# Kernel tuning notes

Hardware: AMD Instinct MI355X
Metric: run time of the kernel (lower is better)

Reference implementation:

```python
import jax, jax.numpy as jnp
import numpy as np

# ---- static config (matches init_kwargs) ----
B, L, C = 32, 512, 32
PRED = 96
D = 256
PS, STRIDE = 16, 8
P = (L - PS) // STRIDE + 1  # 63 patches
H = 4
DH = D // H                 # 64 per head
K = 4                        # causal conv kernel size
NB = 2                       # num sLSTM blocks
UP = 384                     # round_up(1.3 * 256, 64) gated-FFN inner dim


def setup_inputs() -> dict:
    key = jax.random.key(0)
    ks = iter(jax.random.split(key, 32))
    def nrm(shape, s=0.02):
        return jax.random.normal(next(ks), shape, dtype=jnp.float32) * s
    f32 = jnp.float32
    return dict(
        x=jax.random.normal(next(ks), (B, L, C), dtype=f32),
        W_emb=nrm((PS, D)), b_emb=jnp.zeros((D,), f32),
        ln1_w=jnp.ones((NB, D), f32), ln1_b=jnp.zeros((NB, D), f32),
        conv_w=nrm((NB, K, D), 0.1), conv_b=jnp.zeros((NB, D), f32),
        Wg=nrm((NB, 4, H, DH, DH), 0.05),   # input gate projections (i,f,z,o), block-diag per head
        Rg=nrm((NB, 4, H, DH, DH), 0.05),   # recurrent kernels per head
        gb=jnp.zeros((NB, 4, D), f32),      # gate biases
        gn_w=jnp.ones((NB, D), f32),        # per-head groupnorm weight
        ln2_w=jnp.ones((NB, D), f32), ln2_b=jnp.zeros((NB, D), f32),
        up_w=nrm((NB, D, 2 * UP)), up_b=jnp.zeros((NB, 2 * UP), f32),
        dn_w=nrm((NB, UP, D)), dn_b=jnp.zeros((NB, D), f32),
        post_w=jnp.ones((D,), f32), post_b=jnp.zeros((D,), f32),
        W_proj=nrm((D * P, PRED)), b_proj=jnp.zeros((PRED,), f32),
    )


def _layernorm(x, w, b, eps=1e-5):
    mu = x.mean(-1, keepdims=True)
    var = x.var(-1, keepdims=True)
    return (x - mu) / jnp.sqrt(var + eps) * w + b


def _slstm_layer(x, conv_w, conv_b, Wg, Rg, gb, gn_w):
    # x: (N, S, D)
    N, S, _ = x.shape
    # causal depthwise conv (k=K) + swish -> feeds i,f gates
    xp = jnp.pad(x, ((0, 0), (K - 1, 0), (0, 0)))
    xc = sum(xp[:, k:k + S, :] * conv_w[k] for k in range(K)) + conv_b
    xc = xc * jax.nn.sigmoid(xc)
    xh = x.reshape(N, S, H, DH)
    xch = xc.reshape(N, S, H, DH)
    gi = jnp.einsum('nshd,hde->nshe', xch, Wg[0]) + gb[0].reshape(H, DH)
    gf = jnp.einsum('nshd,hde->nshe', xch, Wg[1]) + gb[1].reshape(H, DH)
    gz = jnp.einsum('nshd,hde->nshe', xh, Wg[2]) + gb[2].reshape(H, DH)
    go = jnp.einsum('nshd,hde->nshe', xh, Wg[3]) + gb[3].reshape(H, DH)
    gates = jnp.moveaxis(jnp.stack([gi, gf, gz, go], 0), 2, 0)  # (S, 4, N, H, DH)

    def step(carry, g):
        c, n, h, m = carry  # each (N, H, DH)
        rec = jnp.einsum('nhd,ghde->gnhe', h, Rg)  # (4, N, H, DH)
        ip, fp, zp, op = g[0] + rec[0], g[1] + rec[1], g[2] + rec[2], g[3] + rec[3]
        logf = m + jax.nn.log_sigmoid(fp)          # log(f_t) + m_{t-1}
        m_new = jnp.maximum(ip, logf)              # stabilizer
        i = jnp.exp(ip - m_new)
        f = jnp.exp(logf - m_new)
        c_new = f * c + i * jnp.tanh(zp)
        n_new = f * n + i
        h_new = jax.nn.sigmoid(op) * c_new / n_new
        return (c_new, n_new, h_new, m_new), h_new

    z0 = jnp.zeros((N, H, DH), x.dtype)
    _, hs = jax.lax.scan(step, (z0, z0, z0, z0), gates)
    y = jnp.moveaxis(hs, 0, 1)  # (N, S, H, DH)
    mu = y.mean(-1, keepdims=True)
    var = y.var(-1, keepdims=True)
    y = (y - mu) / jnp.sqrt(var + 1e-5)            # per-head groupnorm
    return y.reshape(N, S, D) * gn_w


def reference(x, W_emb, b_emb, ln1_w, ln1_b, conv_w, conv_b, Wg, Rg, gb, gn_w,
              ln2_w, ln2_b, up_w, up_b, dn_w, dn_b, post_w, post_b, W_proj, b_proj):
    Bb, Ll, Cc = x.shape
    xs = x.transpose(0, 2, 1).reshape(Bb * Cc, Ll)              # (N, L)
    idx = np.arange(P)[:, None] * STRIDE + np.arange(PS)[None, :]
    patches = xs[:, idx]                                         # (N, P, PS) unfold
    h = patches @ W_emb + b_emb                                  # (N, P, D)
    for blk in range(NB):
        h = h + _slstm_layer(_layernorm(h, ln1_w[blk], ln1_b[blk]),
                             conv_w[blk], conv_b[blk], Wg[blk], Rg[blk], gb[blk], gn_w[blk])
        u = _layernorm(h, ln2_w[blk], ln2_b[blk]) @ up_w[blk] + up_b[blk]
        g1, g2 = jnp.split(u, 2, axis=-1)
        h = h + (jax.nn.gelu(g1) * g2) @ dn_w[blk] + dn_b[blk]   # gated FFN
    h = _layernorm(h, post_w, post_b)                            # post-blocks norm
    out = h.reshape(Bb * Cc, D * P) @ W_proj + b_proj            # (N, PRED)
    return out.reshape(Bb, Cc, PRED).transpose(0, 2, 1)          # (B, PRED, C)
```

## Files before the change

### kernel.cpp

```cpp
#include <hip/hip_runtime.h>
#include <stdint.h>

typedef unsigned short u16;
typedef unsigned int   u32;
typedef __attribute__((ext_vector_type(8))) short bf16x8;
typedef __attribute__((ext_vector_type(4))) float f32x4;

#define NS      63
#define NSEQ    1024
#define DDIM    256
#define NHEAD   4
#define DHEAD   64
#define UPDIM   384
#define PREDN   96
#define LLEN    512
#define CCH     32
#define PSIZE   16
#define PSTRIDE 8
#define KC_PROJ 8
#define KCHUNK_PROJ 2016

__device__ __forceinline__ float bf2f(u32 lo16){
  union { u32 i; float f; } v; v.i = lo16 << 16; return v.f;
}
__device__ __forceinline__ float bf2f_hi(u32 u){
  union { u32 i; float f; } v; v.i = u & 0xffff0000u; return v.f;
}
__device__ __forceinline__ u16 f2bf(float f){
  union { u32 i; float f; } v; v.f = f;
  u32 u = v.i; u += 0x7fffu + ((u >> 16) & 1u);
  return (u16)(u >> 16);
}

__device__ __forceinline__ void gload16(const u16* g, u16* lds){
  __builtin_amdgcn_global_load_lds(
      (const __attribute__((address_space(1))) u32*)g,
      (__attribute__((address_space(3))) u32*)lds, 16, 0, 0);
}

template<int N> __device__ __forceinline__ void waitcnt_vm(){
  if constexpr (N == 0) asm volatile("s_waitcnt vmcnt(0)" ::: "memory");
  else if constexpr (N == 4) asm volatile("s_waitcnt vmcnt(4)" ::: "memory");
  else if constexpr (N == 6) asm volatile("s_waitcnt vmcnt(6)" ::: "memory");
}

__device__ __forceinline__ void swz_tile(int &nt, int &mt){
  int gx = gridDim.x, gy = gridDim.y;
  int nwg = gx*gy;
  int flat = blockIdx.y*gx + blockIdx.x;
  int c = flat & 7, s = flat >> 3;
  int q = nwg >> 3, r = nwg & 7;
  int base = c*q + (c < r ? c : r);
  int t = base + s;
  nt = t % gx; mt = t / gx;
}

__global__ __launch_bounds__(256) void cvt_transpose_t(
    const float* __restrict__ src, u16* __restrict__ dst, int R, int C){
  __shared__ u16 tile[32][33];
  int rb = blockIdx.x*32, cb = blockIdx.y*32;
  int tx = threadIdx.x & 31, ty = threadIdx.x >> 5;
  #pragma unroll
  for (int i = ty; i < 32; i += 8){
    int r = rb + i, c = cb + tx;
    tile[i][tx] = (r < R && c < C) ? f2bf(src[(size_t)r*C + c]) : (u16)0;
  }
  __syncthreads();
  #pragma unroll
  for (int i = ty; i < 32; i += 8){
    int c = cb + i, r = rb + tx;
    if (c < C && r < R) dst[(size_t)c*R + r] = tile[tx][i];
  }
}

__global__ __launch_bounds__(256) void cvt_gate(
    const float* __restrict__ src, u16* __restrict__ dst){
  int mat = blockIdx.x, t = threadIdx.x;
  const float* s = src + (size_t)mat*4096;
  u16* d = dst + (size_t)mat*4096;
  for (int i = t; i < 4096; i += 256){
    int r = i >> 6, c = i & 63;
    d[c*64 + r] = f2bf(s[i]);
  }
}

__global__ __launch_bounds__(256) void cvt_gateW2(
    const float* __restrict__ Wg, u16* __restrict__ dst){
  int mi = blockIdx.x;
  int blk = mi >> 3, p = (mi >> 2) & 1, hd = mi & 3;
  u16* d = dst + (size_t)mi*8192;
  for (int i = threadIdx.x; i < 8192; i += 256){
    int n = i >> 6, k = i & 63;
    int e = n >> 1, gl = n & 1;
    int g = 2*p + gl;
    d[i] = f2bf(Wg[((((size_t)blk*4 + g)*4 + hd)*64 + k)*64 + e]);
  }
}

__global__ __launch_bounds__(256) void patch_embed_ln_v(
    const float* __restrict__ x, const float* __restrict__ Wemb,
    const float* __restrict__ bemb, const float* __restrict__ w1,
    const float* __restrict__ b1, u16* __restrict__ h,
    u16* __restrict__ outA, int t_base){
  int wv = blockIdx.x*4 + (threadIdx.x >> 6);
  int lane = threadIdx.x & 63;
  int tg = t_base + wv;
  int n = tg / NS, s = tg - n*NS;
  int b = n >> 5, c = n & 31;
  int l0 = s * PSTRIDE;
  float4 acc = *(const float4*)(bemb + lane*4);
  #pragma unroll
  for (int p = 0; p < PSIZE; ++p){
    float xv = x[((size_t)b*LLEN + l0 + p)*CCH + c];
    float4 we = *(const float4*)(Wemb + p*DDIM + lane*4);
    acc.x += xv*we.x; acc.y += xv*we.y; acc.z += xv*we.z; acc.w += xv*we.w;
  }
  ushort4 hu; hu.x=f2bf(acc.x); hu.y=f2bf(acc.y); hu.z=f2bf(acc.z); hu.w=f2bf(acc.w);
  *(ushort4*)(h + (size_t)wv*DDIM + lane*4) = hu;
  float s1 = acc.x+acc.y+acc.z+acc.w;
  float s2 = acc.x*acc.x+acc.y*acc.y+acc.z*acc.z+acc.w*acc.w;
  #pragma unroll
  for (int o = 1; o < 64; o <<= 1){ s1 += __shfl_xor(s1,o,64); s2 += __shfl_xor(s2,o,64); }
  float mu = s1*(1.f/DDIM);
  float var = s2*(1.f/DDIM) - mu*mu;
  float rstd = rsqrtf(var + 1e-5f);
  float4 wf = *(const float4*)(w1 + lane*4);
  float4 bf = *(const float4*)(b1 + lane*4);
  ushort4 o4;
  o4.x = f2bf((acc.x-mu)*rstd*wf.x + bf.x);
  o4.y = f2bf((acc.y-mu)*rstd*wf.y + bf.y);
  o4.z = f2bf((acc.z-mu)*rstd*wf.z + bf.z);
  o4.w = f2bf((acc.w-mu)*rstd*wf.w + bf.w);
  *(ushort4*)(outA + (size_t)wv*DDIM + lane*4) = o4;
}

__global__ __launch_bounds__(256) void layernorm_v(
    const u16* __restrict__ in, const float* __restrict__ w,
    const float* __restrict__ b, u16* __restrict__ out){
  int wv = blockIdx.x*4 + (threadIdx.x >> 6);
  int lane = threadIdx.x & 63;
  ushort4 u = *(const ushort4*)(in + (size_t)wv*DDIM + lane*4);
  float v0=bf2f(u.x), v1=bf2f(u.y), v2=bf2f(u.z), v3=bf2f(u.w);
  float s1 = v0+v1+v2+v3, s2 = v0*v0+v1*v1+v2*v2+v3*v3;
  #pragma unroll
  for (int o = 1; o < 64; o <<= 1){ s1 += __shfl_xor(s1,o,64); s2 += __shfl_xor(s2,o,64); }
  float mu = s1*(1.f/DDIM);
  float var = s2*(1.f/DDIM) - mu*mu;
  float rstd = rsqrtf(var + 1e-5f);
  float4 wf = *(const float4*)(w + lane*4);
  float4 bf = *(const float4*)(b + lane*4);
  ushort4 o4;
  o4.x = f2bf((v0-mu)*rstd*wf.x + bf.x);
  o4.y = f2bf((v1-mu)*rstd*wf.y + bf.y);
  o4.z = f2bf((v2-mu)*rstd*wf.z + bf.z);
  o4.w = f2bf((v3-mu)*rstd*wf.w + bf.w);
  *(ushort4*)(out + (size_t)wv*DDIM + lane*4) = o4;
}

__global__ __launch_bounds__(256) void gn_res_ln_v(
    const u16* __restrict__ y, const float* __restrict__ gnw,
    const float* __restrict__ w2, const float* __restrict__ b2,
    u16* __restrict__ h, u16* __restrict__ outA){
  int wv = blockIdx.x*4 + (threadIdx.x >> 6);
  int lane = threadIdx.x & 63;
  ushort4 u = *(const ushort4*)(y + (size_t)wv*DDIM + lane*4);
  float v0=bf2f(u.x), v1=bf2f(u.y), v2=bf2f(u.z), v3=bf2f(u.w);
  float s1 = v0+v1+v2+v3, s2 = v0*v0+v1*v1+v2*v2+v3*v3;
  #pragma unroll
  for (int o = 1; o < 16; o <<= 1){ s1 += __shfl_xor(s1,o,64); s2 += __shfl_xor(s2,o,64); }
  float mu64 = s1*(1.f/64.f);
  float var64 = s2*(1.f/64.f) - mu64*mu64;
  float rstd64 = rsqrtf(var64 + 1e-5f);
  float4 gw = *(const float4*)(gnw + lane*4);
  ushort4 hu = *(const ushort4*)(h + (size_t)wv*DDIM + lane*4);
  float h0 = bf2f(hu.x) + (v0-mu64)*rstd64*gw.x;
  float h1 = bf2f(hu.y) + (v1-mu64)*rstd64*gw.y;
  float h2 = bf2f(hu.z) + (v2-mu64)*rstd64*gw.z;
  float h3 = bf2f(hu.w) + (v3-mu64)*rstd64*gw.w;
  ushort4 hn; hn.x=f2bf(h0); hn.y=f2bf(h1); hn.z=f2bf(h2); hn.w=f2bf(h3);
  *(ushort4*)(h + (size_t)wv*DDIM + lane*4) = hn;
  float t1 = h0+h1+h2+h3, t2 = h0*h0+h1*h1+h2*h2+h3*h3;
  #pragma unroll
  for (int o = 1; o < 64; o <<= 1){ t1 += __shfl_xor(t1,o,64); t2 += __shfl_xor(t2,o,64); }
  float mu = t1*(1.f/DDIM);
  float var = t2*(1.f/DDIM) - mu*mu;
  float rstd = rsqrtf(var + 1e-5f);
  float4 wf = *(const float4*)(w2 + lane*4);
  float4 bf = *(const float4*)(b2 + lane*4);
  ushort4 o4;
  o4.x = f2bf((h0-mu)*rstd*wf.x + bf.x);
  o4.y = f2bf((h1-mu)*rstd*wf.y + bf.y);
  o4.z = f2bf((h2-mu)*rstd*wf.z + bf.z);
  o4.w = f2bf((h3-mu)*rstd*wf.w + bf.w);
  *(ushort4*)(outA + (size_t)wv*DDIM + lane*4) = o4;
}

__global__ __launch_bounds__(256) void conv_silu_v(
    const u16* __restrict__ xln, const float* __restrict__ cw,
    const float* __restrict__ cb, u16* __restrict__ xc){
  int wv = blockIdx.x*4 + (threadIdx.x >> 6);
  int lane = threadIdx.x & 63;
  int s = wv % NS;
  float4 acc = *(const float4*)(cb + lane*4);
  #pragma unroll
  for (int k = 0; k < 4; ++k){
    int ss = s + k - 3;
    if (ss >= 0){
      ushort4 xu = *(const ushort4*)(xln + (size_t)(wv + k - 3)*DDIM + lane*4);
      float4 cv = *(const float4*)(cw + k*DDIM + lane*4);
      acc.x += bf2f(xu.x)*cv.x; acc.y += bf2f(xu.y)*cv.y;
      acc.z += bf2f(xu.z)*cv.z; acc.w += bf2f(xu.w)*cv.w;
    }
  }
  ushort4 o4;
  o4.x = f2bf(acc.x/(1.f + __expf(-acc.x)));
  o4.y = f2bf(acc.y/(1.f + __expf(-acc.y)));
  o4.z = f2bf(acc.z/(1.f + __expf(-acc.z)));
  o4.w = f2bf(acc.w/(1.f + __expf(-acc.w)));
  *(ushort4*)(xc + (size_t)wv*DDIM + lane*4) = o4;
}

template<int BM,int BN,int WR,int WC,int MR,int NR,int MODE,int VM>
__global__ __launch_bounds__(256) void mfma_gemm2(
    const u16* __restrict__ A, int lda,
    const u16* __restrict__ Wt, int ldwt,
    const float* __restrict__ bias, void* __restrict__ outp, int ldo,
    int ksteps, int kchunk, int Mtot)
{
  constexpr int nA = BM/16, nW = BN/16;
  __shared__ u16 As[2][BM*32];
  __shared__ u16 Ws[2][BN*32];
  const int tid = threadIdx.x;
  const int lane = tid & 63, wid = tid >> 6;
  const int wr = wid / WC, wc = wid % WC;
  const int fr = lane & 15, kb = lane >> 4;
  int nt, mt; swz_tile(nt, mt);
  const int m0 = mt*BM, n0 = nt*BN;
  const int kc = blockIdx.z;
  const int kbeg = kc*kchunk;
  const u16* Ab = A + (size_t)m0*lda + kbeg;
  const u16* Wb = Wt + (size_t)n0*ldwt + kbeg;
  const int lrow = lane >> 2;
  const int lcol = (((lane & 3) ^ (lrow & 3)) * 8);
  const int rsw = (kb ^ (fr & 3))*8;

  auto stage = [&](int buf, int ks){
    int k0 = ks*32;
    for (int c = wid; c < nA; c += 4)
      gload16(Ab + (size_t)(c*16 + lrow)*lda + k0 + lcol, &As[buf][c*512]);
    for (int c = wid; c < nW; c += 4)
      gload16(Wb + (size_t)(c*16 + lrow)*ldwt + k0 + lcol, &Ws[buf][c*512]);
  };

  f32x4 acc[MR][NR];
  #pragma unroll
  for (int m=0;m<MR;++m)
    #pragma unroll
    for (int n=0;n<NR;++n) acc[m][n] = (f32x4){0.f,0.f,0.f,0.f};

  stage(0, 0);
  if (VM == 0) __syncthreads();
  int cur = 0;
  for (int ks = 0; ks < ksteps; ++ks){
    if (VM == 0){
      if (ks + 1 < ksteps) stage(cur^1, ks+1);
    } else {
      if (ks + 1 < ksteps){ stage(cur^1, ks+1); waitcnt_vm<VM>(); }
      else waitcnt_vm<0>();
      __builtin_amdgcn_s_barrier();
      asm volatile("" ::: "memory");
    }
    bf16x8 af[MR], wf[NR];
    #pragma unroll
    for (int m=0;m<MR;++m)
      af[m] = *(const bf16x8*)&As[cur][(wr*MR*16 + m*16 + fr)*32 + rsw];
    #pragma unroll
    for (int n=0;n<NR;++n)
      wf[n] = *(const bf16x8*)&Ws[cur][(wc*NR*16 + n*16 + fr)*32 + rsw];
    #pragma unroll
    for (int m=0;m<MR;++m)
      #pragma unroll
      for (int n=0;n<NR;++n)
        acc[m][n] = __builtin_amdgcn_mfma_f32_16x16x32_bf16(af[m], wf[n], acc[m][n], 0,0,0);
    if (VM == 0){
      __syncthreads();
    } else {
      asm volatile("" ::: "memory");
      __builtin_amdgcn_s_barrier();
    }
    cur ^= 1;
  }
  #pragma unroll
  for (int m=0;m<MR;++m){
    int rowb = m0 + wr*MR*16 + m*16 + kb*4;
    #pragma unroll
    for (int n=0;n<NR;++n){
      int col = n0 + wc*NR*16 + n*16 + fr;
      #pragma unroll
      for (int r=0;r<4;++r){
        int row = rowb + r;
        float v = acc[m][n][r];
        if (MODE == 1){
          u16* dst = (u16*)outp + (size_t)row*ldo + col;
          *dst = f2bf(bf2f(*dst) + v + bias[col]);
        } else {
          ((float*)outp)[((size_t)kc*Mtot + row)*ldo + col] = v;
        }
      }
    }
  }
}

__global__ __launch_bounds__(256) void mfma_gate2(
    const u16* __restrict__ xc, const u16* __restrict__ xh,
    const u16* __restrict__ Wg2, const float* __restrict__ gb,
    u16* __restrict__ gates)
{
  __shared__ u16 As[2][128*32];
  __shared__ u16 Ws[2][128*32];
  const int tid = threadIdx.x;
  const int lane = tid & 63, wid = tid >> 6;
  const int wr = wid >> 1, wc = wid & 1;
  const int fr = lane & 15, kb = lane >> 4;
  int nt, mt; swz_tile(nt, mt);
  const int p = nt >> 2, hd = nt & 3;
  const int m0 = mt*128;
  const u16* Ain = (p == 0) ? xc : xh;
  const u16* Wb = Wg2 + (size_t)nt*8192;
  const int lrow = lane >> 2;
  const int lcol = (((lane & 3) ^ (lrow & 3)) * 8);
  const int rsw = (kb ^ (fr & 3))*8;

  auto stage = [&](int buf, int ks){
    int k0 = ks*32;
    for (int c = wid; c < 8; c += 4)
      gload16(Ain + (size_t)(m0 + c*16 + lrow)*DDIM + hd*64 + k0 + lcol, &As[buf][c*512]);
    for (int c = wid; c < 8; c += 4)
      gload16(Wb + (size_t)(c*16 + lrow)*64 + k0 + lcol, &Ws[buf][c*512]);
  };

  f32x4 acc[4][4];
  #pragma unroll
  for (int m=0;m<4;++m)
    #pragma unroll
    for (int n=0;n<4;++n) acc[m][n] = (f32x4){0.f,0.f,0.f,0.f};

  stage(0, 0);
  int cur = 0;
  #pragma unroll
  for (int ks = 0; ks < 2; ++ks){
    if (ks == 0){ stage(1, 1); waitcnt_vm<4>(); }
    else waitcnt_vm<0>();
    __builtin_amdgcn_s_barrier();
    asm volatile("" ::: "memory");
    bf16x8 af[4], wf[4];
    #pragma unroll
    for (int m=0;m<4;++m)
      af[m] = *(const bf16x8*)&As[cur][(wr*64 + m*16 + fr)*32 + rsw];
    #pragma unroll
    for (int n=0;n<4;++n)
      wf[n] = *(const bf16x8*)&Ws[cur][(wc*64 + n*16 + fr)*32 + rsw];
    #pragma unroll
    for (int m=0;m<4;++m)
      #pragma unroll
      for (int n=0;n<4;++n)
        acc[m][n] = __builtin_amdgcn_mfma_f32_16x16x32_bf16(af[m], wf[n], acc[m][n], 0,0,0);
    asm volatile("" ::: "memory");
    __builtin_amdgcn_s_barrier();
    cur ^= 1;
  }
  #pragma unroll
  for (int m=0;m<4;++m){
    int rowb = m0 + wr*64 + m*16 + kb*4;
    #pragma unroll
    for (int n=0;n<4;++n){
      int cl = wc*64 + n*16 + fr;
      int e = cl >> 1, gl = cl & 1;
      float bv = gb[(2*p + gl)*256 + hd*64 + e];
      int phys = hd*256 + p*128 + cl;
      #pragma unroll
      for (int r=0;r<4;++r)
        gates[(size_t)(rowb + r)*1024 + phys] = f2bf(acc[m][n][r] + bv);
    }
  }
}

__global__ __launch_bounds__(256) void mfma_up_gelu3(
    const u16* __restrict__ A, const u16* __restrict__ Wt,
    const float* __restrict__ ub, u16* __restrict__ gp)
{
  __shared__ u16 As[2][256*32];
  __shared__ u16 Ws[2][128*32];
  const int tid = threadIdx.x;
  const int lane = tid & 63, wid = tid >> 6;
  const int fr = lane & 15, kb = lane >> 4;
  int nt, mt; swz_tile(nt, mt);
  const int m0 = mt*256, n0 = nt*64;
  const u16* W1 = Wt + (size_t)n0*256;
  const u16* W2 = Wt + (size_t)(384 + n0)*256;
  const int lrow = lane >> 2;
  const int lcol = (((lane & 3) ^ (lrow & 3)) * 8);
  const int rsw = (kb ^ (fr & 3))*8;

  auto stage = [&](int buf, int ks){
    int k0 = ks*32;
    for (int c = wid; c < 16; c += 4)
      gload16(A + (size_t)(m0 + c*16 + lrow)*256 + k0 + lcol, &As[buf][c*512]);
    for (int c = wid; c < 8; c += 4){
      const u16* src = (c < 4) ? (W1 + (size_t)(c*16 + lrow)*256)
                               : (W2 + (size_t)((c-4)*16 + lrow)*256);
      gload16(src + k0 + lcol, &Ws[buf][c*512]);
    }
  };

  f32x4 a1[4][4], a2[4][4];
  #pragma unroll
  for (int m=0;m<4;++m)
    #pragma unroll
    for (int n=0;n<4;++n){ a1[m][n]=(f32x4){0,0,0,0}; a2[m][n]=(f32x4){0,0,0,0}; }

  stage(0, 0);
  int cur = 0;
  #pragma unroll
  for (int ks = 0; ks < 8; ++ks){
    if (ks + 1 < 8){ stage(cur^1, ks+1); waitcnt_vm<6>(); }
    else waitcnt_vm<0>();
    __builtin_amdgcn_s_barrier();
    asm volatile("" ::: "memory");
    bf16x8 af[4], wf1[4], wf2[4];
    #pragma unroll
    for (int m=0;m<4;++m)
      af[m] = *(const bf16x8*)&As[cur][(wid*64 + m*16 + fr)*32 + rsw];
    #pragma unroll
    for (int n=0;n<4;++n){
      wf1[n] = *(const bf16x8*)&Ws[cur][(n*16 + fr)*32 + rsw];
      wf2[n] = *(const bf16x8*)&Ws[cur][(64 + n*16 + fr)*32 + rsw];
    }
    #pragma unroll
    for (int m=0;m<4;++m)
      #pragma unroll
      for (int n=0;n<4;++n){
        a1[m][n] = __builtin_amdgcn_mfma_f32_16x16x32_bf16(af[m], wf1[n], a1[m][n], 0,0,0);
        a2[m][n] = __builtin_amdgcn_mfma_f32_16x16x32_bf16(af[m], wf2[n], a2[m][n], 0,0,0);
      }
    asm volatile("" ::: "memory");
    __builtin_amdgcn_s_barrier();
    cur ^= 1;
  }
  #pragma unroll
  for (int m=0;m<4;++m){
    int rowb = m0 + wid*64 + m*16 + kb*4;
    #pragma unroll
    for (int n=0;n<4;++n){
      int col = n0 + n*16 + fr;
      float b1 = ub[col], b2 = ub[384 + col];
      #pragma unroll
      for (int r=0;r<4;++r){
        float g1 = a1[m][n][r] + b1;
        float g2 = a2[m][n][r] + b2;
        float u  = 0.7978845608028654f*(g1 + 0.044715f*g1*g1*g1);
        float uc = fminf(fmaxf(u, -20.f), 20.f);
        float t2 = __expf(uc + uc);
        float th = (t2 - 1.f)/(t2 + 1.f);
        float ge = 0.5f*g1*(1.f + th);
        gp[(size_t)(rowb + r)*UPDIM + col] = f2bf(ge*g2);
      }
    }
  }
}

__global__ __launch_bounds__(256) void slstm_scan4(
    const u16* __restrict__ gates, const u16* __restrict__ Rgt,
    u16* __restrict__ y)
{
  __shared__ u16 h_lds[16*72];
  __shared__ float rec_lds[4][16][68];
  const int tid = threadIdx.x;
  const int w = tid >> 6, lane = tid & 63;
  const int hd = blockIdx.y, grp = blockIdx.x;
  const int fr = lane & 15, kb = lane >> 4;
  const int seq0 = grp*16;
  const u32* g32 = (const u32*)gates;

  bf16x8 bfr[4][2];
  {
    const u16* rb = Rgt + (size_t)(w*NHEAD + hd)*4096;
    #pragma unroll
    for (int n=0;n<4;++n)
      #pragma unroll
      for (int ks=0;ks<2;++ks)
        bfr[n][ks] = *(const bf16x8*)(rb + (size_t)(n*16 + fr)*64 + ks*32 + kb*8);
  }
  for (int i = tid; i < 16*72/2; i += 256) ((u32*)h_lds)[i] = 0u;
  float c[4]={0,0,0,0}, nst[4]={0,0,0,0}, m[4]={0,0,0,0};

  size_t gb4[4];
  #pragma unroll
  for (int si=0; si<4; ++si)
    gb4[si] = ((size_t)(seq0 + 4*w + si)*NS)*512 + hd*128 + lane;

  u32 g0[4][2], g1[4][2];
  #pragma unroll
  for (int si=0; si<4; ++si){
    g0[si][0] = g32[gb4[si]];        g0[si][1] = g32[gb4[si] + 64];
    g1[si][0] = g32[gb4[si] + 512];  g1[si][1] = g32[gb4[si] + 576];
  }
  __syncthreads();

  for (int s = 0; s < NS; ++s){
    u32 gn[4][2] = {};
    if (s + 2 < NS){
      #pragma unroll
      for (int si=0; si<4; ++si){
        size_t b2 = gb4[si] + (size_t)(s+2)*512;
        gn[si][0] = g32[b2];
        gn[si][1] = g32[b2 + 64];
      }
    }
    bf16x8 af0 = *(const bf16x8*)&h_lds[fr*72 + kb*8];
    bf16x8 af1 = *(const bf16x8*)&h_lds[fr*72 + 32 + kb*8];
    f32x4 acc[4];
    #pragma unroll
    for (int n=0;n<4;++n){
      acc[n] = (f32x4){0,0,0,0};
      acc[n] = __builtin_amdgcn_mfma_f32_16x16x32_bf16(af0, bfr[n][0], acc[n], 0,0,0);
      acc[n] = __builtin_amdgcn_mfma_f32_16x16x32_bf16(af1, bfr[n][1], acc[n], 0,0,0);
    }
    #pragma unroll
    for (int n=0;n<4;++n)
      #pragma unroll
      for (int r=0;r<4;++r)
        rec_lds[w][kb*4 + r][n*16 + fr] = acc[n][r];
    asm volatile("s_waitcnt lgkmcnt(0)" ::: "memory");
    __builtin_amdgcn_s_barrier();
    #pragma unroll
    for (int si=0; si<4; ++si){
      int sidx = 4*w + si;
      float ip = rec_lds[0][sidx][lane] + bf2f(g0[si][0] & 0xffffu);
      float fp = rec_lds[1][sidx][lane] + bf2f_hi(g0[si][0]);
      float zp = rec_lds[2][sidx][lane] + bf2f(g0[si][1] & 0xffffu);
      float op = rec_lds[3][sidx][lane] + bf2f_hi(g0[si][1]);
      float sp  = __logf(1.f + __expf(-fabsf(fp)));
      float lg  = m[si] + fminf(fp, 0.f) - sp;
      float mn  = fmaxf(ip, lg);
      float iv  = __expf(ip - mn);
      float fv  = __expf(lg - mn);
      float zz  = fminf(fabsf(zp), 15.f);
      float t2  = __expf(zz + zz);
      float tha = (t2 - 1.f)/(t2 + 1.f);
      float th  = (zp >= 0.f) ? tha : -tha;
      c[si]   = fv*c[si] + iv*th;
      nst[si] = fv*nst[si] + iv;
      m[si]   = mn;
      float hv = c[si] * __builtin_amdgcn_rcpf(nst[si]*(1.f + __expf(-op)));
      h_lds[sidx*72 + lane] = f2bf(hv);
      size_t t = (size_t)(seq0 + sidx)*NS + s;
      y[t*DDIM + hd*64 + lane] = f2bf(hv);
    }
    asm volatile("s_waitcnt lgkmcnt(0)" ::: "memory");
    __builtin_amdgcn_s_barrier();
    #pragma unroll
    for (int si=0; si<4; ++si){
      g0[si][0] = g1[si][0]; g0[si][1] = g1[si][1];
      g1[si][0] = gn[si][0]; g1[si][1] = gn[si][1];
    }
  }
}

__global__ __launch_bounds__(256) void proj_out(
    const float* __restrict__ ptmp, const float* __restrict__ bproj,
    float* __restrict__ out, int Nc, int n0glob){
  int gid = blockIdx.x*256 + threadIdx.x;
  if (gid >= Nc*PREDN) return;
  float acc = 0.f;
  #pragma unroll
  for (int kc = 0; kc < KC_PROJ; ++kc) acc += ptmp[(size_t)kc*Nc*PREDN + gid];
  int nl = gid / PREDN, j = gid - nl*PREDN;
  int n = n0glob + nl;
  out[((size_t)(n >> 5)*PREDN + j)*CCH + (n & 31)] = acc + bproj[j];
}

extern "C" void kernel_launch(void* const* d_in, const int* in_sizes, int n_in,
                              void* d_out, int out_size, void* d_ws, size_t ws_size,
                              hipStream_t stream) {
  const float* x      = (const float*)d_in[0];
  const float* W_emb  = (const float*)d_in[1];
  const float* b_emb  = (const float*)d_in[2];
  const float* ln1_w  = (const float*)d_in[3];
  const float* ln1_b  = (const float*)d_in[4];
  const float* conv_w = (const float*)d_in[5];
  const float* conv_b = (const float*)d_in[6];
  const float* Wg     = (const float*)d_in[7];
  const float* Rg     = (const float*)d_in[8];
  const float* gb     = (const float*)d_in[9];
  const float* gn_w   = (const float*)d_in[10];
  const float* ln2_w  = (const float*)d_in[11];
  const float* ln2_b  = (const float*)d_in[12];
  const float* up_w   = (const float*)d_in[13];
  const float* up_b   = (const float*)d_in[14];
  const float* dn_w   = (const float*)d_in[15];
  const float* dn_b   = (const float*)d_in[16];
  const float* post_w = (const float*)d_in[17];
  const float* post_b = (const float*)d_in[18];
  const float* W_proj = (const float*)d_in[19];
  const float* b_proj = (const float*)d_in[20];
  float* out = (float*)d_out;

  const size_t oWu   = 0;
  const size_t oWd   = 1572864;
  const size_t oWg2  = 2359296;
  const size_t oRgt  = 2621440;
  const size_t oWp   = 3145728;
  const size_t oChunk = 6242304;
  const size_t per_seq = (size_t)3584*NS;
  int Nc = 0;
  const int cands[3] = {1024, 512, 256};
  for (int i = 0; i < 3; ++i)
    if (oChunk + (size_t)cands[i]*per_seq <= ws_size){ Nc = cands[i]; break; }
  if (Nc == 0) return;

  char* wsb = (char*)d_ws;
  u16* Wu   = (u16*)(wsb + oWu);
  u16* Wd   = (u16*)(wsb + oWd);
  u16* Wg2  = (u16*)(wsb + oWg2);
  u16* Rgt  = (u16*)(wsb + oRgt);
  u16* Wtp  = (u16*)(wsb + oWp);

  for (int blk = 0; blk < 2; ++blk){
    cvt_transpose_t<<<dim3(8, 24), 256, 0, stream>>>(
        up_w + (size_t)blk*256*768, Wu + (size_t)blk*768*256, 256, 768);
    cvt_transpose_t<<<dim3(12, 8), 256, 0, stream>>>(
        dn_w + (size_t)blk*384*256, Wd + (size_t)blk*256*384, 384, 256);
  }
  cvt_gateW2<<<16, 256, 0, stream>>>(Wg, Wg2);
  cvt_gate<<<32, 256, 0, stream>>>(Rg, Rgt);
  cvt_transpose_t<<<dim3(504, 3), 256, 0, stream>>>(W_proj, Wtp, 16128, 96);

  for (int n0 = 0; n0 < NSEQ; n0 += Nc){
    const int    nc  = (NSEQ - n0 < Nc) ? (NSEQ - n0) : Nc;
    const size_t Tc  = (size_t)nc * NS;
    char* cb = wsb + oChunk;
    u16*   h_c   = (u16*)cb;
    u16*   bufA  = (u16*)(cb + Tc*512);
    u16*   bufB  = (u16*)(cb + Tc*1024);
    u16*   gates = (u16*)(cb + Tc*1536);
    u16*   gp    = gates;
    float* ptmp  = (float*)(cb + Tc*1536 + Tc*1024);
    const int t_base = n0*NS;
    const int Tci = (int)Tc;

    patch_embed_ln_v<<<Tci/4, 256, 0, stream>>>(
        x, W_emb, b_emb, ln1_w, ln1_b, h_c, bufA, t_base);

    for (int blk = 0; blk < 2; ++blk){
      if (blk == 1)
        layernorm_v<<<Tci/4, 256, 0, stream>>>(h_c, ln1_w + DDIM, ln1_b + DDIM, bufA);
      conv_silu_v<<<Tci/4, 256, 0, stream>>>(bufA, conv_w + blk*4*DDIM, conv_b + blk*DDIM, bufB);
      mfma_gate2<<<dim3(8, Tci/128), 256, 0, stream>>>(
          bufB, bufA, Wg2 + (size_t)blk*8*8192, gb + blk*4*DDIM, gates);
      slstm_scan4<<<dim3(nc/16, NHEAD), 256, 0, stream>>>(
          gates, Rgt + (size_t)blk*16*4096, bufB);
      gn_res_ln_v<<<Tci/4, 256, 0, stream>>>(
          bufB, gn_w + blk*DDIM, ln2_w + blk*DDIM, ln2_b + blk*DDIM, h_c, bufA);
      mfma_up_gelu3<<<dim3(6, Tci/256), 256, 0, stream>>>(
          bufA, Wu + (size_t)blk*768*256, up_b + blk*2*UPDIM, gp);
      mfma_gemm2<256,128,4,1,4,8,1,6><<<dim3(2, Tci/256), 256, 0, stream>>>(
          gp, UPDIM, Wd + (size_t)blk*256*384, UPDIM,
          dn_b + blk*DDIM, (void*)h_c, DDIM, 12, 0, 0);
    }

    layernorm_v<<<Tci/4, 256, 0, stream>>>(h_c, post_w, post_b, bufA);
    mfma_gemm2<64,96,2,2,2,3,2,0><<<dim3(1, nc/64, KC_PROJ), 256, 0, stream>>>(
        bufA, NS*DDIM, Wtp, NS*DDIM,
        b_proj, (void*)ptmp, PREDN, KCHUNK_PROJ/32, KCHUNK_PROJ, nc);
    proj_out<<<(nc*PREDN + 255)/256, 256, 0, stream>>>(ptmp, b_proj, out, nc, n0);
  }
}
```

Before: 731.9 us.

## Shrink sLSTM scan block to four sequences for more parallel blocks

The recurrent scan kernel now handles 4 sequences per block (one per wavefront) instead of 16, and launches four times as many blocks. Each wave does one sequence's pointwise update instead of four, which shortens the serial per-step latency and spreads the scan across more CUs. The cost is that the MFMA tiles are mostly padding: 16-row tiles now hold only 4 real rows, so recurrent matmul work per useful row grows fourfold. Recurrent weights are also reloaded by four times as many blocks.

```diff
diff --git a/kernel.cpp b/kernel.cpp
--- a/kernel.cpp
+++ b/kernel.cpp
@@ -469,17 +469,17 @@
   }
 }
 
-__global__ __launch_bounds__(256) void slstm_scan4(
+__global__ __launch_bounds__(256) void slstm_scan5(
     const u16* __restrict__ gates, const u16* __restrict__ Rgt,
     u16* __restrict__ y)
 {
   __shared__ u16 h_lds[16*72];
-  __shared__ float rec_lds[4][16][68];
+  __shared__ float rec_lds[4][4][68];
   const int tid = threadIdx.x;
   const int w = tid >> 6, lane = tid & 63;
   const int hd = blockIdx.y, grp = blockIdx.x;
   const int fr = lane & 15, kb = lane >> 4;
-  const int seq0 = grp*16;
+  const int seq0 = grp*4;
   const u32* g32 = (const u32*)gates;
 
   bf16x8 bfr[4][2];
@@ -492,30 +492,20 @@
         bfr[n][ks] = *(const bf16x8*)(rb + (size_t)(n*16 + fr)*64 + ks*32 + kb*8);
   }
   for (int i = tid; i < 16*72/2; i += 256) ((u32*)h_lds)[i] = 0u;
-  float c[4]={0,0,0,0}, nst[4]={0,0,0,0}, m[4]={0,0,0,0};
-
-  size_t gb4[4];
-  #pragma unroll
-  for (int si=0; si<4; ++si)
-    gb4[si] = ((size_t)(seq0 + 4*w + si)*NS)*512 + hd*128 + lane;
-
-  u32 g0[4][2], g1[4][2];
-  #pragma unroll
-  for (int si=0; si<4; ++si){
-    g0[si][0] = g32[gb4[si]];        g0[si][1] = g32[gb4[si] + 64];
-    g1[si][0] = g32[gb4[si] + 512];  g1[si][1] = g32[gb4[si] + 576];
-  }
+  float c = 0.f, nst = 0.f, m = 0.f;
+
+  const size_t gb = ((size_t)(seq0 + w)*NS)*512 + hd*128 + lane;
+  u32 g0[2], g1[2];
+  g0[0] = g32[gb];        g0[1] = g32[gb + 64];
+  g1[0] = g32[gb + 512];  g1[1] = g32[gb + 576];
   __syncthreads();
 
   for (int s = 0; s < NS; ++s){
-    u32 gn[4][2] = {};
+    u32 gn[2] = {0u, 0u};
     if (s + 2 < NS){
-      #pragma unroll
-      for (int si=0; si<4; ++si){
-        size_t b2 = gb4[si] + (size_t)(s+2)*512;
-        gn[si][0] = g32[b2];
-        gn[si][1] = g32[b2 + 64];
-      }
+      size_t b2 = gb + (size_t)(s+2)*512;
+      gn[0] = g32[b2];
+      gn[1] = g32[b2 + 64];
     }
     bf16x8 af0 = *(const bf16x8*)&h_lds[fr*72 + kb*8];
     bf16x8 af1 = *(const bf16x8*)&h_lds[fr*72 + 32 + kb*8];
@@ -526,22 +516,22 @@
       acc[n] = __builtin_amdgcn_mfma_f32_16x16x32_bf16(af0, bfr[n][0], acc[n], 0,0,0);
       acc[n] = __builtin_amdgcn_mfma_f32_16x16x32_bf16(af1, bfr[n][1], acc[n], 0,0,0);
     }
-    #pragma unroll
-    for (int n=0;n<4;++n)
-      #pragma unroll
-      for (int r=0;r<4;++r)
-        rec_lds[w][kb*4 + r][n*16 + fr] = acc[n][r];
+    if (kb == 0){
+      #pragma unroll
+      for (int n=0;n<4;++n)
+        #pragma unroll
+        for (int r=0;r<4;++r)
+          rec_lds[w][r][n*16 + fr] = acc[n][r];
+    }
     asm volatile("s_waitcnt lgkmcnt(0)" ::: "memory");
     __builtin_amdgcn_s_barrier();
-    #pragma unroll
-    for (int si=0; si<4; ++si){
-      int sidx = 4*w + si;
-      float ip = rec_lds[0][sidx][lane] + bf2f(g0[si][0] & 0xffffu);
-      float fp = rec_lds[1][sidx][lane] + bf2f_hi(g0[si][0]);
-      float zp = rec_lds[2][sidx][lane] + bf2f(g0[si][1] & 0xffffu);
-      float op = rec_lds[3][sidx][lane] + bf2f_hi(g0[si][1]);
+    {
+      float ip = rec_lds[0][w][lane] + bf2f(g0[0] & 0xffffu);
+      float fp = rec_lds[1][w][lane] + bf2f_hi(g0[0]);
+      float zp = rec_lds[2][w][lane] + bf2f(g0[1] & 0xffffu);
+      float op = rec_lds[3][w][lane] + bf2f_hi(g0[1]);
       float sp  = __logf(1.f + __expf(-fabsf(fp)));
-      float lg  = m[si] + fminf(fp, 0.f) - sp;
+      float lg  = m + fminf(fp, 0.f) - sp;
       float mn  = fmaxf(ip, lg);
       float iv  = __expf(ip - mn);
       float fv  = __expf(lg - mn);
@@ -549,21 +539,18 @@
       float t2  = __expf(zz + zz);
       float tha = (t2 - 1.f)/(t2 + 1.f);
       float th  = (zp >= 0.f) ? tha : -tha;
-      c[si]   = fv*c[si] + iv*th;
-      nst[si] = fv*nst[si] + iv;
-      m[si]   = mn;
-      float hv = c[si] * __builtin_amdgcn_rcpf(nst[si]*(1.f + __expf(-op)));
-      h_lds[sidx*72 + lane] = f2bf(hv);
-      size_t t = (size_t)(seq0 + sidx)*NS + s;
+      c   = fv*c + iv*th;
+      nst = fv*nst + iv;
+      m   = mn;
+      float hv = c * __builtin_amdgcn_rcpf(nst*(1.f + __expf(-op)));
+      h_lds[w*72 + lane] = f2bf(hv);
+      size_t t = (size_t)(seq0 + w)*NS + s;
       y[t*DDIM + hd*64 + lane] = f2bf(hv);
     }
     asm volatile("s_waitcnt lgkmcnt(0)" ::: "memory");
     __builtin_amdgcn_s_barrier();
-    #pragma unroll
-    for (int si=0; si<4; ++si){
-      g0[si][0] = g1[si][0]; g0[si][1] = g1[si][1];
-      g1[si][0] = gn[si][0]; g1[si][1] = gn[si][1];
-    }
+    g0[0] = g1[0]; g0[1] = g1[1];
+    g1[0] = gn[0]; g1[1] = gn[1];
   }
 }
 
@@ -658,7 +645,7 @@
       conv_silu_v<<<Tci/4, 256, 0, stream>>>(bufA, conv_w + blk*4*DDIM, conv_b + blk*DDIM, bufB);
       mfma_gate2<<<dim3(8, Tci/128), 256, 0, stream>>>(
           bufB, bufA, Wg2 + (size_t)blk*8*8192, gb + blk*4*DDIM, gates);
-      slstm_scan4<<<dim3(nc/16, NHEAD), 256, 0, stream>>>(
+      slstm_scan5<<<dim3(nc/4, NHEAD), 256, 0, stream>>>(
           gates, Rgt + (size_t)blk*16*4096, bufB);
       gn_res_ln_v<<<Tci/4, 256, 0, stream>>>(
           bufB, gn_w + blk*DDIM, ln2_w + blk*DDIM, ln2_b + blk*DDIM, h_c, bufA);
```

Measured after the change: 706.5 us. 1.04x faster.
